# Optimization experiments

Hardware: AMD Instinct MI355X
Metric: run time of the kernel (lower is better)

## Reference

```python
import math
import jax, jax.numpy as jnp
import numpy as np

BS, Q_LEN, DIM = 8, 16, 4096
MAX_SEQ = 4096
N_Q_HEADS, N_KV_HEADS, HEAD_DIM = 32, 8, 128
REP = N_Q_HEADS // N_KV_HEADS


def setup_inputs() -> dict:
    key = jax.random.key(0)
    ks = jax.random.split(key, 12)
    w = 0.02
    return {
        "x": jax.random.normal(ks[0], (BS, Q_LEN, DIM), jnp.float32),
        "k_cache": jax.random.normal(ks[1], (BS, MAX_SEQ, N_KV_HEADS, HEAD_DIM), jnp.float32),
        "v_cache": jax.random.normal(ks[2], (BS, MAX_SEQ, N_KV_HEADS, HEAD_DIM), jnp.float32),
        "Wq": jax.random.normal(ks[3], (DIM, N_Q_HEADS * HEAD_DIM), jnp.float32) * w,
        "bq": jax.random.normal(ks[4], (N_Q_HEADS * HEAD_DIM,), jnp.float32) * w,
        "Wk": jax.random.normal(ks[5], (DIM, N_KV_HEADS * HEAD_DIM), jnp.float32) * w,
        "bk": jax.random.normal(ks[6], (N_KV_HEADS * HEAD_DIM,), jnp.float32) * w,
        "Wv": jax.random.normal(ks[7], (DIM, N_KV_HEADS * HEAD_DIM), jnp.float32) * w,
        "bv": jax.random.normal(ks[8], (N_KV_HEADS * HEAD_DIM,), jnp.float32) * w,
        "Wo": jax.random.normal(ks[9], (N_Q_HEADS * HEAD_DIM, DIM), jnp.float32) * w,
        "bo": jax.random.normal(ks[10], (DIM,), jnp.float32) * w,
        "start_pos": MAX_SEQ - Q_LEN,
        "seq_len_for_kv": Q_LEN,
    }


def reference(x, k_cache, v_cache, Wq, bq, Wk, bk, Wv, bv, Wo, bo, start_pos, seq_len_for_kv):
    bs, sl, dim = x.shape
    # Projections (torch Linear: x @ W^T + b; here W stored as [in, out])
    q = (x @ Wq + bq).reshape(bs, sl, N_KV_HEADS, REP, HEAD_DIM)  # [b, q, g, r, d]
    k = (x @ Wk + bk).reshape(bs, sl, N_KV_HEADS, HEAD_DIM)
    v = (x @ Wv + bv).reshape(bs, sl, N_KV_HEADS, HEAD_DIM)
    # KV-cache append (start_pos / seq_len_for_kv are static Python ints)
    k_cache = k_cache.at[:, start_pos:start_pos + seq_len_for_kv].set(k)
    v_cache = v_cache.at[:, start_pos:start_pos + seq_len_for_kv].set(v)
    kv_len = start_pos + seq_len_for_kv
    keys = k_cache[:, :kv_len]    # [b, L, g, d]
    vals = v_cache[:, :kv_len]    # [b, L, g, d]
    # GQA: each kv head g serves REP query heads r (broadcast instead of repeat_kv)
    scale = 1.0 / math.sqrt(HEAD_DIM)
    scores = jnp.einsum('bqgrd,blgd->bgrql', q, keys) * scale  # [b, g, r, q, L]
    att = jax.nn.softmax(scores, axis=-1)
    out = jnp.einsum('bgrql,blgd->bqgrd', att, vals)           # [b, q, g, r, d]
    out = out.reshape(bs, sl, N_Q_HEADS * HEAD_DIM)
    return out @ Wo + bo
```

## Files before the change

kernel.cpp:

```cpp
#include <hip/hip_runtime.h>
#include <math.h>

#define DIM       4096
#define NKVH      8
#define HD        128
#define MAX_SEQ   4096
#define START_POS 4080
#define NQKV      6144
#define NCHUNK    8
#define CHUNK     512
#define ATT_SCALE 0.08838834764831845f

#define WS_PART   0
#define WS_QH     3145728
#define WS_QL     3407872
#define WS_KNEW   3670016
#define WS_VNEW   3801088
#define WS_PARTO  3932160
#define WS_PM     8126464
#define WS_PL     8159232
#define WS_ATH    8192000
#define WS_ATL    8454144
#define WS_XH     WS_PARTO
#define WS_XL     (WS_PARTO + 262144)

typedef __bf16 bf16x8 __attribute__((ext_vector_type(8)));
typedef float  f32x4  __attribute__((ext_vector_type(4)));
typedef unsigned int uintx4 __attribute__((ext_vector_type(4)));

__device__ __forceinline__ unsigned short f2bf(float f) {
    union { float f; unsigned int u; } v; v.f = f;
    unsigned int r = v.u + 0x7FFFu + ((v.u >> 16) & 1u);
    return (unsigned short)(r >> 16);
}
__device__ __forceinline__ float bf2f(unsigned short h) {
    union { unsigned int u; float f; } v; v.u = ((unsigned int)h) << 16;
    return v.f;
}
__device__ __forceinline__ void splitbf(float f, unsigned short &h, unsigned short &l) {
    h = f2bf(f);
    l = f2bf(f - bf2f(h));
}
__device__ __forceinline__ bf16x8 ldsfrag(const unsigned short* p) {
    uintx4 u = *(const uintx4*)p;
    return __builtin_bit_cast(bf16x8, u);
}
#define MFMA16(a,b,c) __builtin_amdgcn_mfma_f32_16x16x32_bf16(a, b, c, 0, 0, 0)

__global__ __launch_bounds__(256) void split_x_kernel(
    const float* __restrict__ x, unsigned short* __restrict__ xh,
    unsigned short* __restrict__ xl, int n)
{
    int i = blockIdx.x * 256 + threadIdx.x;
    if (i < n) { unsigned short h, l; splitbf(x[i], h, l); xh[i] = h; xl[i] = l; }
}

__device__ __forceinline__ void gemm_body(
    const unsigned short* __restrict__ Ah, const unsigned short* __restrict__ Al,
    const float* __restrict__ W, int ldW, int noff,
    float* __restrict__ part, int partStride, int ncol0, int ks,
    unsigned short* Ahs, unsigned short* Als,
    unsigned short* Bhs, unsigned short* Bls)
{
    const int t = threadIdx.x;
    const int w = t >> 6, lane = t & 63, l15 = lane & 15, quad = lane >> 4;
    f32x4 acc[2][4];
    #pragma unroll
    for (int i = 0; i < 2; ++i)
        #pragma unroll
        for (int nt = 0; nt < 4; ++nt) acc[i][nt] = (f32x4){0.f, 0.f, 0.f, 0.f};

    const int k0base = ks * 1024;
    uintx4 areg_h[4], areg_l[4];
    float4 wreg[4];

    auto LOAD = [&](int it) {
        int k0 = k0base + it * 64;
        #pragma unroll
        for (int i = 0; i < 4; ++i) {
            int f = t + i * 256;
            int row = f >> 3, c0 = (f & 7) << 3;
            size_t off = (size_t)row * DIM + k0 + c0;
            areg_h[i] = *(const uintx4*)(Ah + off);
            areg_l[i] = *(const uintx4*)(Al + off);
        }
        #pragma unroll
        for (int i = 0; i < 4; ++i) {
            int f = t + i * 256;
            int kk = f >> 4, n0 = (f & 15) << 2;
            wreg[i] = *(const float4*)(W + (size_t)(k0 + kk) * ldW + noff + n0);
        }
    };

    LOAD(0);
    for (int it = 0; it < 16; ++it) {
        __syncthreads();
        #pragma unroll
        for (int i = 0; i < 4; ++i) {
            int f = t + i * 256;
            int row = f >> 3, c0 = (f & 7) << 3;
            *(uintx4*)(Ahs + row * 72 + c0) = areg_h[i];
            *(uintx4*)(Als + row * 72 + c0) = areg_l[i];
        }
        #pragma unroll
        for (int i = 0; i < 4; ++i) {
            int f = t + i * 256;
            int kk = f >> 4, n0 = (f & 15) << 2;
            float vv[4] = {wreg[i].x, wreg[i].y, wreg[i].z, wreg[i].w};
            #pragma unroll
            for (int j = 0; j < 4; ++j) {
                unsigned short h, l; splitbf(vv[j], h, l);
                Bhs[(n0 + j) * 72 + kk] = h;
                Bls[(n0 + j) * 72 + kk] = l;
            }
        }
        __syncthreads();
        if (it < 15) LOAD(it + 1);
        #pragma unroll
        for (int kt = 0; kt < 2; ++kt) {
            int ko = kt * 32 + quad * 8;
            bf16x8 ah0 = ldsfrag(Ahs + ((2*w+0)*16 + l15) * 72 + ko);
            bf16x8 ah1 = ldsfrag(Ahs + ((2*w+1)*16 + l15) * 72 + ko);
            bf16x8 al0 = ldsfrag(Als + ((2*w+0)*16 + l15) * 72 + ko);
            bf16x8 al1 = ldsfrag(Als + ((2*w+1)*16 + l15) * 72 + ko);
            #pragma unroll
            for (int nt = 0; nt < 4; ++nt) {
                bf16x8 bh = ldsfrag(Bhs + (nt*16 + l15) * 72 + ko);
                bf16x8 bl = ldsfrag(Bls + (nt*16 + l15) * 72 + ko);
                acc[0][nt] = MFMA16(ah0, bh, acc[0][nt]);
                acc[0][nt] = MFMA16(ah0, bl, acc[0][nt]);
                acc[0][nt] = MFMA16(al0, bh, acc[0][nt]);
                acc[1][nt] = MFMA16(ah1, bh, acc[1][nt]);
                acc[1][nt] = MFMA16(ah1, bl, acc[1][nt]);
                acc[1][nt] = MFMA16(al1, bh, acc[1][nt]);
            }
        }
    }
    #pragma unroll
    for (int i = 0; i < 2; ++i)
        #pragma unroll
        for (int nt = 0; nt < 4; ++nt)
            #pragma unroll
            for (int r = 0; r < 4; ++r) {
                int row = (2*w + i) * 16 + quad * 4 + r;
                int col = ncol0 + nt * 16 + l15;
                part[(size_t)(ks * 128 + row) * partStride + col] = acc[i][nt][r];
            }
}

__global__ __launch_bounds__(256) void qkv_gemm_kernel(
    const unsigned short* __restrict__ xh, const unsigned short* __restrict__ xl,
    const float* __restrict__ Wq, const float* __restrict__ Wk,
    const float* __restrict__ Wv, float* __restrict__ part)
{
    __shared__ unsigned short Ahs[128 * 72], Als[128 * 72];
    __shared__ unsigned short Bhs[64 * 72],  Bls[64 * 72];
    int ncol0 = blockIdx.x * 64;
    int ks = blockIdx.y;
    const float* W; int ldW, noff;
    if (ncol0 < 4096)      { W = Wq; ldW = 4096; noff = ncol0; }
    else if (ncol0 < 5120) { W = Wk; ldW = 1024; noff = ncol0 - 4096; }
    else                   { W = Wv; ldW = 1024; noff = ncol0 - 5120; }
    gemm_body(xh, xl, W, ldW, noff, part, NQKV, ncol0, ks, Ahs, Als, Bhs, Bls);
}

__global__ __launch_bounds__(256) void oproj_gemm_kernel(
    const unsigned short* __restrict__ ah, const unsigned short* __restrict__ al,
    const float* __restrict__ Wo, float* __restrict__ part)
{
    __shared__ unsigned short Ahs[128 * 72], Als[128 * 72];
    __shared__ unsigned short Bhs[64 * 72],  Bls[64 * 72];
    int ncol0 = blockIdx.x * 64;
    int ks = blockIdx.y;
    gemm_body(ah, al, Wo, 4096, ncol0, part, 4096, ncol0, ks, Ahs, Als, Bhs, Bls);
}

__global__ __launch_bounds__(256) void qkv_reduce_kernel(
    const float* __restrict__ part, const float* __restrict__ bq,
    const float* __restrict__ bk, const float* __restrict__ bv,
    unsigned short* __restrict__ qh, unsigned short* __restrict__ ql,
    float* __restrict__ k_new, float* __restrict__ v_new)
{
    int gid = blockIdx.x * 256 + threadIdx.x;
    int row = gid / NQKV;
    int n   = gid - row * NQKV;
    float s = part[(size_t)row * NQKV + n]
            + part[(size_t)(128 + row) * NQKV + n]
            + part[(size_t)(256 + row) * NQKV + n]
            + part[(size_t)(384 + row) * NQKV + n];
    if (n < 4096) {
        float v = s + bq[n];
        unsigned short h, l; splitbf(v, h, l);
        qh[row * 4096 + n] = h; ql[row * 4096 + n] = l;
    } else if (n < 5120) k_new[row * 1024 + (n - 4096)] = s + bk[n - 4096];
    else                 v_new[row * 1024 + (n - 5120)] = s + bv[n - 5120];
}

__global__ __launch_bounds__(256) void attn_partial2_kernel(
    const unsigned short* __restrict__ qhp, const unsigned short* __restrict__ qlp,
    const float* __restrict__ kc, const float* __restrict__ vc,
    const float* __restrict__ knew, const float* __restrict__ vnew,
    float* __restrict__ part_O, float* __restrict__ part_m, float* __restrict__ part_l)
{
    __shared__ unsigned short Kh[32 * 136], Kl[32 * 136];
    __shared__ unsigned short Vh[128 * 40], Vl[128 * 40];
    __shared__ unsigned short Ph[4 * 16 * 40], Pl[4 * 16 * 40];
    const int t = threadIdx.x;
    const int w = t >> 6, lane = t & 63, l15 = lane & 15, quad = lane >> 4;
    const int blk = blockIdx.x;
    const int b = blk >> 6, g = (blk >> 3) & 7, c = blk & 7;

    bf16x8 qhf[4], qlf[4];
    {
        size_t base = (size_t)(b * 16 + l15) * DIM + (g * 4 + w) * HD + quad * 8;
        #pragma unroll
        for (int kt = 0; kt < 4; ++kt) {
            qhf[kt] = ldsfrag(qhp + base + kt * 32);
            qlf[kt] = ldsfrag(qlp + base + kt * 32);
        }
    }

    float m_run[4], l_run[4];
    f32x4 oacc[8];
    #pragma unroll
    for (int r = 0; r < 4; ++r) { m_run[r] = -INFINITY; l_run[r] = 0.f; }
    #pragma unroll
    for (int d = 0; d < 8; ++d) oacc[d] = (f32x4){0.f, 0.f, 0.f, 0.f};

    float4 kreg[4], vreg[4];
    auto LOADKV = [&](int it) {
        #pragma unroll
        for (int i = 0; i < 4; ++i) {
            int f = t + i * 256;
            int pos = f >> 5, d0 = (f & 31) << 2;
            int pg = c * CHUNK + it * 32 + pos;
            const float *ksrc, *vsrc;
            if (pg >= START_POS) {
                size_t off = (size_t)(b * 16 + pg - START_POS) * (NKVH * HD) + g * HD + d0;
                ksrc = knew + off; vsrc = vnew + off;
            } else {
                size_t off = ((size_t)(b * MAX_SEQ + pg) * NKVH + g) * HD + d0;
                ksrc = kc + off; vsrc = vc + off;
            }
            kreg[i] = *(const float4*)ksrc;
            vreg[i] = *(const float4*)vsrc;
        }
    };

    unsigned short* phw = Ph + w * 640;
    unsigned short* plw = Pl + w * 640;

    LOADKV(0);
    for (int it = 0; it < CHUNK / 32; ++it) {
        __syncthreads();
        #pragma unroll
        for (int i = 0; i < 4; ++i) {
            int f = t + i * 256;
            int pos = f >> 5, d0 = (f & 31) << 2;
            float kv[4] = {kreg[i].x, kreg[i].y, kreg[i].z, kreg[i].w};
            float vv[4] = {vreg[i].x, vreg[i].y, vreg[i].z, vreg[i].w};
            unsigned short h0,l0,h1,l1,h2,l2,h3,l3;
            splitbf(kv[0],h0,l0); splitbf(kv[1],h1,l1);
            splitbf(kv[2],h2,l2); splitbf(kv[3],h3,l3);
            *(ushort4*)&Kh[pos * 136 + d0] = make_ushort4(h0,h1,h2,h3);
            *(ushort4*)&Kl[pos * 136 + d0] = make_ushort4(l0,l1,l2,l3);
            #pragma unroll
            for (int j = 0; j < 4; ++j) {
                unsigned short h, l; splitbf(vv[j], h, l);
                Vh[(d0 + j) * 40 + pos] = h;
                Vl[(d0 + j) * 40 + pos] = l;
            }
        }
        __syncthreads();
        if (it + 1 < CHUNK / 32) LOADKV(it + 1);

        f32x4 sacc[2];
        sacc[0] = (f32x4){0.f,0.f,0.f,0.f};
        sacc[1] = (f32x4){0.f,0.f,0.f,0.f};
        #pragma unroll
        for (int nt = 0; nt < 2; ++nt)
            #pragma unroll
            for (int kt = 0; kt < 4; ++kt) {
                const unsigned short* kp = &Kh[(nt*16 + l15) * 136 + kt*32 + quad*8];
                const unsigned short* lp = &Kl[(nt*16 + l15) * 136 + kt*32 + quad*8];
                bf16x8 bh = ldsfrag(kp), bl = ldsfrag(lp);
                sacc[nt] = MFMA16(qhf[kt], bh, sacc[nt]);
                sacc[nt] = MFMA16(qhf[kt], bl, sacc[nt]);
                sacc[nt] = MFMA16(qlf[kt], bh, sacc[nt]);
            }

        float e0[4], e1[4], alpha[4];
        #pragma unroll
        for (int r = 0; r < 4; ++r) {
            float s0 = sacc[0][r] * ATT_SCALE;
            float s1 = sacc[1][r] * ATT_SCALE;
            float mx = fmaxf(s0, s1);
            mx = fmaxf(mx, __shfl_xor(mx, 1));
            mx = fmaxf(mx, __shfl_xor(mx, 2));
            mx = fmaxf(mx, __shfl_xor(mx, 4));
            mx = fmaxf(mx, __shfl_xor(mx, 8));
            float mnew = fmaxf(m_run[r], mx);
            alpha[r] = __expf(m_run[r] - mnew);
            e0[r] = __expf(s0 - mnew);
            e1[r] = __expf(s1 - mnew);
            float sum = e0[r] + e1[r];
            sum += __shfl_xor(sum, 1);
            sum += __shfl_xor(sum, 2);
            sum += __shfl_xor(sum, 4);
            sum += __shfl_xor(sum, 8);
            l_run[r] = l_run[r] * alpha[r] + sum;
            m_run[r] = mnew;
        }
        #pragma unroll
        for (int d = 0; d < 8; ++d)
            #pragma unroll
            for (int r = 0; r < 4; ++r) oacc[d][r] *= alpha[r];

        #pragma unroll
        for (int r = 0; r < 4; ++r) {
            unsigned short h, l;
            splitbf(e0[r], h, l);
            phw[(quad*4 + r) * 40 + l15] = h;
            plw[(quad*4 + r) * 40 + l15] = l;
            splitbf(e1[r], h, l);
            phw[(quad*4 + r) * 40 + 16 + l15] = h;
            plw[(quad*4 + r) * 40 + 16 + l15] = l;
        }
        bf16x8 pah = ldsfrag(phw + l15 * 40 + quad * 8);
        bf16x8 pal = ldsfrag(plw + l15 * 40 + quad * 8);

        #pragma unroll
        for (int d = 0; d < 8; ++d) {
            bf16x8 vh = ldsfrag(&Vh[(d*16 + l15) * 40 + quad * 8]);
            bf16x8 vl = ldsfrag(&Vl[(d*16 + l15) * 40 + quad * 8]);
            oacc[d] = MFMA16(pah, vh, oacc[d]);
            oacc[d] = MFMA16(pah, vl, oacc[d]);
            oacc[d] = MFMA16(pal, vh, oacc[d]);
        }
    }

    #pragma unroll
    for (int d = 0; d < 8; ++d)
        #pragma unroll
        for (int r = 0; r < 4; ++r)
            part_O[((size_t)blk * 64 + w * 16 + quad * 4 + r) * HD + d * 16 + l15] = oacc[d][r];
    if (l15 == 0) {
        #pragma unroll
        for (int r = 0; r < 4; ++r) {
            part_m[blk * 64 + w * 16 + quad * 4 + r] = m_run[r];
            part_l[blk * 64 + w * 16 + quad * 4 + r] = l_run[r];
        }
    }
}

__global__ __launch_bounds__(128) void attn_combine_kernel(
    const float* __restrict__ part_O, const float* __restrict__ part_m,
    const float* __restrict__ part_l, unsigned short* __restrict__ ah,
    unsigned short* __restrict__ al)
{
    int bid = blockIdx.x;
    int d = threadIdx.x;
    int bg = bid >> 6;
    int row = bid & 63;
    float mc[NCHUNK], lc[NCHUNK];
    float M = -INFINITY;
    #pragma unroll
    for (int cc = 0; cc < NCHUNK; ++cc) {
        mc[cc] = part_m[(bg * NCHUNK + cc) * 64 + row];
        lc[cc] = part_l[(bg * NCHUNK + cc) * 64 + row];
        M = fmaxf(M, mc[cc]);
    }
    float L = 0.f, acc = 0.f;
    #pragma unroll
    for (int cc = 0; cc < NCHUNK; ++cc) {
        float wgt = __expf(mc[cc] - M);
        L += lc[cc] * wgt;
        acc += part_O[((size_t)(bg * NCHUNK + cc) * 64 + row) * HD + d] * wgt;
    }
    int b = bg >> 3, g = bg & 7;
    int r = row >> 4, qp = row & 15;
    float v = acc / L;
    unsigned short h, l; splitbf(v, h, l);
    size_t idx = (size_t)(b * 16 + qp) * DIM + (g * 4 + r) * HD + d;
    ah[idx] = h; al[idx] = l;
}

__global__ __launch_bounds__(256) void oproj_reduce_kernel(
    const float* __restrict__ part, const float* __restrict__ bo,
    float* __restrict__ out)
{
    int gid = blockIdx.x * 256 + threadIdx.x;
    int n = gid & 4095;
    float s = part[gid] + part[524288 + gid] + part[1048576 + gid] + part[1572864 + gid];
    out[gid] = s + bo[n];
}

extern "C" void kernel_launch(void* const* d_in, const int* in_sizes, int n_in,
                              void* d_out, int out_size, void* d_ws, size_t ws_size,
                              hipStream_t stream)
{
    const float* x  = (const float*)d_in[0];
    const float* kc = (const float*)d_in[1];
    const float* vc = (const float*)d_in[2];
    const float* Wq = (const float*)d_in[3];
    const float* bq = (const float*)d_in[4];
    const float* Wk = (const float*)d_in[5];
    const float* bk = (const float*)d_in[6];
    const float* Wv = (const float*)d_in[7];
    const float* bv = (const float*)d_in[8];
    const float* Wo = (const float*)d_in[9];
    const float* bo = (const float*)d_in[10];
    float* out = (float*)d_out;
    float* ws  = (float*)d_ws;

    unsigned short* xh = (unsigned short*)(ws + WS_XH);
    unsigned short* xl = (unsigned short*)(ws + WS_XL);
    unsigned short* qh = (unsigned short*)(ws + WS_QH);
    unsigned short* ql = (unsigned short*)(ws + WS_QL);
    unsigned short* ath = (unsigned short*)(ws + WS_ATH);
    unsigned short* atl = (unsigned short*)(ws + WS_ATL);

    split_x_kernel<<<2048, 256, 0, stream>>>(x, xh, xl, 524288);
    qkv_gemm_kernel<<<dim3(96, 4), 256, 0, stream>>>(xh, xl, Wq, Wk, Wv, ws + WS_PART);
    qkv_reduce_kernel<<<3072, 256, 0, stream>>>(ws + WS_PART, bq, bk, bv,
                                                qh, ql, ws + WS_KNEW, ws + WS_VNEW);
    attn_partial2_kernel<<<512, 256, 0, stream>>>(qh, ql, kc, vc,
                                                  ws + WS_KNEW, ws + WS_VNEW,
                                                  ws + WS_PARTO, ws + WS_PM, ws + WS_PL);
    attn_combine_kernel<<<4096, 128, 0, stream>>>(ws + WS_PARTO, ws + WS_PM,
                                                  ws + WS_PL, ath, atl);
    oproj_gemm_kernel<<<dim3(64, 4), 256, 0, stream>>>(ath, atl, Wo, ws + WS_PART);
    oproj_reduce_kernel<<<2048, 256, 0, stream>>>(ws + WS_PART, bo, out);
}
```

Before: 495.9 us.

## Drop low-bf16 split of weights and K/V, double split-K, repack LDS layouts

The B operand (weights, K cache and V cache) is now rounded to a single bf16 instead of a hi/lo pair. This removes one third of the MFMAs in the projection GEMMs and the attention, and halves the LDS traffic for those operands. The split-K factor for both GEMMs goes from 4 to 8, which doubles the grid and halves the K loop per block, at the cost of more partial-sum traffic in the reduce kernels. The workspace offsets are reorganised, the V and P LDS tiles use a packed transposed layout with vector stores, and accuracy drops because the bf16 error of weights and cache values is no longer corrected.

```diff
diff --git a/kernel.cpp b/kernel.cpp
--- a/kernel.cpp
+++ b/kernel.cpp
@@ -9,20 +9,21 @@
 #define NQKV      6144
 #define NCHUNK    8
 #define CHUNK     512
+#define KS        8
 #define ATT_SCALE 0.08838834764831845f
 
 #define WS_PART   0
-#define WS_QH     3145728
-#define WS_QL     3407872
-#define WS_KNEW   3670016
-#define WS_VNEW   3801088
-#define WS_PARTO  3932160
-#define WS_PM     8126464
-#define WS_PL     8159232
-#define WS_ATH    8192000
-#define WS_ATL    8454144
-#define WS_XH     WS_PARTO
-#define WS_XL     (WS_PARTO + 262144)
+#define WS_QH     6291456
+#define WS_QL     6553600
+#define WS_KNEW   6815744
+#define WS_VNEW   6946816
+#define WS_PM     7077888
+#define WS_PL     7110656
+#define WS_ATH    7143424
+#define WS_ATL    7405568
+#define WS_XH     7667712
+#define WS_XL     7929856
+#define WS_PARTO  WS_PART
 
 typedef __bf16 bf16x8 __attribute__((ext_vector_type(8)));
 typedef float  f32x4  __attribute__((ext_vector_type(4)));
@@ -45,7 +46,14 @@
     uintx4 u = *(const uintx4*)p;
     return __builtin_bit_cast(bf16x8, u);
 }
+__device__ __forceinline__ bf16x8 ldsfrag2(const unsigned short* p) {
+    union { uint2 u2[2]; bf16x8 v; } u;
+    u.u2[0] = *(const uint2*)p;
+    u.u2[1] = *(const uint2*)(p + 4);
+    return u.v;
+}
 #define MFMA16(a,b,c) __builtin_amdgcn_mfma_f32_16x16x32_bf16(a, b, c, 0, 0, 0)
+#define VCOMP(v,j) ((j)==0?(v).x:((j)==1?(v).y:((j)==2?(v).z:(v).w)))
 
 __global__ __launch_bounds__(256) void split_x_kernel(
     const float* __restrict__ x, unsigned short* __restrict__ xh,
@@ -59,8 +67,7 @@
     const unsigned short* __restrict__ Ah, const unsigned short* __restrict__ Al,
     const float* __restrict__ W, int ldW, int noff,
     float* __restrict__ part, int partStride, int ncol0, int ks,
-    unsigned short* Ahs, unsigned short* Als,
-    unsigned short* Bhs, unsigned short* Bls)
+    unsigned short* Ahs, unsigned short* Als, unsigned short* Bs)
 {
     const int t = threadIdx.x;
     const int w = t >> 6, lane = t & 63, l15 = lane & 15, quad = lane >> 4;
@@ -70,7 +77,7 @@
         #pragma unroll
         for (int nt = 0; nt < 4; ++nt) acc[i][nt] = (f32x4){0.f, 0.f, 0.f, 0.f};
 
-    const int k0base = ks * 1024;
+    const int k0base = ks * 512;
     uintx4 areg_h[4], areg_l[4];
     float4 wreg[4];
 
@@ -86,14 +93,14 @@
         }
         #pragma unroll
         for (int i = 0; i < 4; ++i) {
-            int f = t + i * 256;
-            int kk = f >> 4, n0 = (f & 15) << 2;
+            int kk = (t >> 4) + 16 * i;
+            int n0 = (t & 15) << 2;
             wreg[i] = *(const float4*)(W + (size_t)(k0 + kk) * ldW + noff + n0);
         }
     };
 
     LOAD(0);
-    for (int it = 0; it < 16; ++it) {
+    for (int it = 0; it < 8; ++it) {
         __syncthreads();
         #pragma unroll
         for (int i = 0; i < 4; ++i) {
@@ -102,20 +109,18 @@
             *(uintx4*)(Ahs + row * 72 + c0) = areg_h[i];
             *(uintx4*)(Als + row * 72 + c0) = areg_l[i];
         }
-        #pragma unroll
-        for (int i = 0; i < 4; ++i) {
-            int f = t + i * 256;
-            int kk = f >> 4, n0 = (f & 15) << 2;
-            float vv[4] = {wreg[i].x, wreg[i].y, wreg[i].z, wreg[i].w};
-            #pragma unroll
-            for (int j = 0; j < 4; ++j) {
-                unsigned short h, l; splitbf(vv[j], h, l);
-                Bhs[(n0 + j) * 72 + kk] = h;
-                Bls[(n0 + j) * 72 + kk] = l;
+        {
+            int n0 = (t & 15) << 2;
+            #pragma unroll
+            for (int i = 0; i < 4; ++i) {
+                int kk = (t >> 4) + 16 * i;
+                #pragma unroll
+                for (int j = 0; j < 4; ++j)
+                    Bs[(n0 + j) * 68 + kk] = f2bf(VCOMP(wreg[i], j));
             }
         }
         __syncthreads();
-        if (it < 15) LOAD(it + 1);
+        if (it < 7) LOAD(it + 1);
         #pragma unroll
         for (int kt = 0; kt < 2; ++kt) {
             int ko = kt * 32 + quad * 8;
@@ -125,14 +130,11 @@
             bf16x8 al1 = ldsfrag(Als + ((2*w+1)*16 + l15) * 72 + ko);
             #pragma unroll
             for (int nt = 0; nt < 4; ++nt) {
-                bf16x8 bh = ldsfrag(Bhs + (nt*16 + l15) * 72 + ko);
-                bf16x8 bl = ldsfrag(Bls + (nt*16 + l15) * 72 + ko);
-                acc[0][nt] = MFMA16(ah0, bh, acc[0][nt]);
-                acc[0][nt] = MFMA16(ah0, bl, acc[0][nt]);
-                acc[0][nt] = MFMA16(al0, bh, acc[0][nt]);
-                acc[1][nt] = MFMA16(ah1, bh, acc[1][nt]);
-                acc[1][nt] = MFMA16(ah1, bl, acc[1][nt]);
-                acc[1][nt] = MFMA16(al1, bh, acc[1][nt]);
+                bf16x8 b = ldsfrag2(Bs + (nt*16 + l15) * 68 + ko);
+                acc[0][nt] = MFMA16(ah0, b, acc[0][nt]);
+                acc[0][nt] = MFMA16(al0, b, acc[0][nt]);
+                acc[1][nt] = MFMA16(ah1, b, acc[1][nt]);
+                acc[1][nt] = MFMA16(al1, b, acc[1][nt]);
             }
         }
     }
@@ -154,14 +156,14 @@
     const float* __restrict__ Wv, float* __restrict__ part)
 {
     __shared__ unsigned short Ahs[128 * 72], Als[128 * 72];
-    __shared__ unsigned short Bhs[64 * 72],  Bls[64 * 72];
+    __shared__ unsigned short Bs[64 * 68];
     int ncol0 = blockIdx.x * 64;
     int ks = blockIdx.y;
     const float* W; int ldW, noff;
     if (ncol0 < 4096)      { W = Wq; ldW = 4096; noff = ncol0; }
     else if (ncol0 < 5120) { W = Wk; ldW = 1024; noff = ncol0 - 4096; }
     else                   { W = Wv; ldW = 1024; noff = ncol0 - 5120; }
-    gemm_body(xh, xl, W, ldW, noff, part, NQKV, ncol0, ks, Ahs, Als, Bhs, Bls);
+    gemm_body(xh, xl, W, ldW, noff, part, NQKV, ncol0, ks, Ahs, Als, Bs);
 }
 
 __global__ __launch_bounds__(256) void oproj_gemm_kernel(
@@ -169,10 +171,10 @@
     const float* __restrict__ Wo, float* __restrict__ part)
 {
     __shared__ unsigned short Ahs[128 * 72], Als[128 * 72];
-    __shared__ unsigned short Bhs[64 * 72],  Bls[64 * 72];
+    __shared__ unsigned short Bs[64 * 68];
     int ncol0 = blockIdx.x * 64;
     int ks = blockIdx.y;
-    gemm_body(ah, al, Wo, 4096, ncol0, part, 4096, ncol0, ks, Ahs, Als, Bhs, Bls);
+    gemm_body(ah, al, Wo, 4096, ncol0, part, 4096, ncol0, ks, Ahs, Als, Bs);
 }
 
 __global__ __launch_bounds__(256) void qkv_reduce_kernel(
@@ -184,10 +186,10 @@
     int gid = blockIdx.x * 256 + threadIdx.x;
     int row = gid / NQKV;
     int n   = gid - row * NQKV;
-    float s = part[(size_t)row * NQKV + n]
-            + part[(size_t)(128 + row) * NQKV + n]
-            + part[(size_t)(256 + row) * NQKV + n]
-            + part[(size_t)(384 + row) * NQKV + n];
+    float s = 0.f;
+    #pragma unroll
+    for (int j = 0; j < KS; ++j)
+        s += part[(size_t)(j * 128 + row) * NQKV + n];
     if (n < 4096) {
         float v = s + bq[n];
         unsigned short h, l; splitbf(v, h, l);
@@ -196,15 +198,15 @@
     else                 v_new[row * 1024 + (n - 5120)] = s + bv[n - 5120];
 }
 
-__global__ __launch_bounds__(256) void attn_partial2_kernel(
+__global__ __launch_bounds__(256) void attn_partial3_kernel(
     const unsigned short* __restrict__ qhp, const unsigned short* __restrict__ qlp,
     const float* __restrict__ kc, const float* __restrict__ vc,
     const float* __restrict__ knew, const float* __restrict__ vnew,
     float* __restrict__ part_O, float* __restrict__ part_m, float* __restrict__ part_l)
 {
-    __shared__ unsigned short Kh[32 * 136], Kl[32 * 136];
-    __shared__ unsigned short Vh[128 * 40], Vl[128 * 40];
-    __shared__ unsigned short Ph[4 * 16 * 40], Pl[4 * 16 * 40];
+    __shared__ unsigned short Kb[32 * 136];
+    __shared__ unsigned short Vt[128 * 36];
+    __shared__ unsigned short Pw[4 * 16 * 36];
     const int t = threadIdx.x;
     const int w = t >> 6, lane = t & 63, l15 = lane & 15, quad = lane >> 4;
     const int blk = blockIdx.x;
@@ -247,8 +249,7 @@
         }
     };
 
-    unsigned short* phw = Ph + w * 640;
-    unsigned short* plw = Pl + w * 640;
+    unsigned short* phw = Pw + w * 576;
 
     LOADKV(0);
     for (int it = 0; it < CHUNK / 32; ++it) {
@@ -257,18 +258,17 @@
         for (int i = 0; i < 4; ++i) {
             int f = t + i * 256;
             int pos = f >> 5, d0 = (f & 31) << 2;
-            float kv[4] = {kreg[i].x, kreg[i].y, kreg[i].z, kreg[i].w};
-            float vv[4] = {vreg[i].x, vreg[i].y, vreg[i].z, vreg[i].w};
-            unsigned short h0,l0,h1,l1,h2,l2,h3,l3;
-            splitbf(kv[0],h0,l0); splitbf(kv[1],h1,l1);
-            splitbf(kv[2],h2,l2); splitbf(kv[3],h3,l3);
-            *(ushort4*)&Kh[pos * 136 + d0] = make_ushort4(h0,h1,h2,h3);
-            *(ushort4*)&Kl[pos * 136 + d0] = make_ushort4(l0,l1,l2,l3);
+            ushort4 k4 = make_ushort4(f2bf(kreg[i].x), f2bf(kreg[i].y),
+                                      f2bf(kreg[i].z), f2bf(kreg[i].w));
+            *(ushort4*)&Kb[pos * 136 + d0] = k4;
+        }
+        {
+            int p0 = t >> 5, d0 = (t & 31) << 2;
             #pragma unroll
             for (int j = 0; j < 4; ++j) {
-                unsigned short h, l; splitbf(vv[j], h, l);
-                Vh[(d0 + j) * 40 + pos] = h;
-                Vl[(d0 + j) * 40 + pos] = l;
+                ushort4 v4 = make_ushort4(f2bf(VCOMP(vreg[0], j)), f2bf(VCOMP(vreg[1], j)),
+                                          f2bf(VCOMP(vreg[2], j)), f2bf(VCOMP(vreg[3], j)));
+                *(ushort4*)&Vt[(d0 + j) * 36 + p0 * 4] = v4;
             }
         }
         __syncthreads();
@@ -281,11 +281,8 @@
         for (int nt = 0; nt < 2; ++nt)
             #pragma unroll
             for (int kt = 0; kt < 4; ++kt) {
-                const unsigned short* kp = &Kh[(nt*16 + l15) * 136 + kt*32 + quad*8];
-                const unsigned short* lp = &Kl[(nt*16 + l15) * 136 + kt*32 + quad*8];
-                bf16x8 bh = ldsfrag(kp), bl = ldsfrag(lp);
+                bf16x8 bh = ldsfrag(&Kb[(nt*16 + l15) * 136 + kt*32 + quad*8]);
                 sacc[nt] = MFMA16(qhf[kt], bh, sacc[nt]);
-                sacc[nt] = MFMA16(qhf[kt], bl, sacc[nt]);
                 sacc[nt] = MFMA16(qlf[kt], bh, sacc[nt]);
             }
 
@@ -316,34 +313,28 @@
             #pragma unroll
             for (int r = 0; r < 4; ++r) oacc[d][r] *= alpha[r];
 
-        #pragma unroll
-        for (int r = 0; r < 4; ++r) {
-            unsigned short h, l;
-            splitbf(e0[r], h, l);
-            phw[(quad*4 + r) * 40 + l15] = h;
-            plw[(quad*4 + r) * 40 + l15] = l;
-            splitbf(e1[r], h, l);
-            phw[(quad*4 + r) * 40 + 16 + l15] = h;
-            plw[(quad*4 + r) * 40 + 16 + l15] = l;
-        }
-        bf16x8 pah = ldsfrag(phw + l15 * 40 + quad * 8);
-        bf16x8 pal = ldsfrag(plw + l15 * 40 + quad * 8);
-
-        #pragma unroll
-        for (int d = 0; d < 8; ++d) {
-            bf16x8 vh = ldsfrag(&Vh[(d*16 + l15) * 40 + quad * 8]);
-            bf16x8 vl = ldsfrag(&Vl[(d*16 + l15) * 40 + quad * 8]);
-            oacc[d] = MFMA16(pah, vh, oacc[d]);
-            oacc[d] = MFMA16(pah, vl, oacc[d]);
-            oacc[d] = MFMA16(pal, vh, oacc[d]);
-        }
-    }
-
-    #pragma unroll
-    for (int d = 0; d < 8; ++d)
+        {
+            int slot0 = 4 * (l15 & 7) + (l15 >> 3);
+            #pragma unroll
+            for (int r = 0; r < 4; ++r) {
+                phw[(quad*4 + r) * 36 + slot0]     = f2bf(e0[r]);
+                phw[(quad*4 + r) * 36 + slot0 + 2] = f2bf(e1[r]);
+            }
+        }
+        bf16x8 pa = ldsfrag(phw + l15 * 36 + quad * 8);
+
+        #pragma unroll
+        for (int dt = 0; dt < 8; ++dt) {
+            bf16x8 vb = ldsfrag(&Vt[(dt*16 + l15) * 36 + quad * 8]);
+            oacc[dt] = MFMA16(pa, vb, oacc[dt]);
+        }
+    }
+
+    #pragma unroll
+    for (int dt = 0; dt < 8; ++dt)
         #pragma unroll
         for (int r = 0; r < 4; ++r)
-            part_O[((size_t)blk * 64 + w * 16 + quad * 4 + r) * HD + d * 16 + l15] = oacc[d][r];
+            part_O[((size_t)blk * 64 + w * 16 + quad * 4 + r) * HD + dt * 16 + l15] = oacc[dt][r];
     if (l15 == 0) {
         #pragma unroll
         for (int r = 0; r < 4; ++r) {
@@ -391,7 +382,9 @@
 {
     int gid = blockIdx.x * 256 + threadIdx.x;
     int n = gid & 4095;
-    float s = part[gid] + part[524288 + gid] + part[1048576 + gid] + part[1572864 + gid];
+    float s = 0.f;
+    #pragma unroll
+    for (int j = 0; j < KS; ++j) s += part[(size_t)j * 524288 + gid];
     out[gid] = s + bo[n];
 }
 
@@ -421,14 +414,14 @@
     unsigned short* atl = (unsigned short*)(ws + WS_ATL);
 
     split_x_kernel<<<2048, 256, 0, stream>>>(x, xh, xl, 524288);
-    qkv_gemm_kernel<<<dim3(96, 4), 256, 0, stream>>>(xh, xl, Wq, Wk, Wv, ws + WS_PART);
+    qkv_gemm_kernel<<<dim3(96, KS), 256, 0, stream>>>(xh, xl, Wq, Wk, Wv, ws + WS_PART);
     qkv_reduce_kernel<<<3072, 256, 0, stream>>>(ws + WS_PART, bq, bk, bv,
                                                 qh, ql, ws + WS_KNEW, ws + WS_VNEW);
-    attn_partial2_kernel<<<512, 256, 0, stream>>>(qh, ql, kc, vc,
+    attn_partial3_kernel<<<512, 256, 0, stream>>>(qh, ql, kc, vc,
                                                   ws + WS_KNEW, ws + WS_VNEW,
                                                   ws + WS_PARTO, ws + WS_PM, ws + WS_PL);
     attn_combine_kernel<<<4096, 128, 0, stream>>>(ws + WS_PARTO, ws + WS_PM,
                                                   ws + WS_PL, ath, atl);
-    oproj_gemm_kernel<<<dim3(64, 4), 256, 0, stream>>>(ath, atl, Wo, ws + WS_PART);
+    oproj_gemm_kernel<<<dim3(64, KS), 256, 0, stream>>>(ath, atl, Wo, ws + WS_PART);
     oproj_reduce_kernel<<<2048, 256, 0, stream>>>(ws + WS_PART, bo, out);
 }
```

New measurement: 435.5 us. 12.2% less time.
